# Performance work log

Hardware: AMD Instinct MI355X
Metric: run time of the kernel (lower is better)

## Reference

```python
import jax, jax.numpy as jnp
import numpy as np

B, N, C, G = 32, 1024, 64, 64

def setup_inputs() -> dict:
    key = jax.random.key(0)
    ks = jax.random.split(key, 8)
    return {
        "x": jax.random.normal(ks[0], (B, N, C), dtype=jnp.float32),
        "valid_len": jax.random.randint(ks[1], (B,), 0, N, dtype=jnp.int64) if jax.config.jax_enable_x64 else jax.random.randint(ks[1], (B,), 0, N, dtype=jnp.int32),
        "Wq": jax.random.normal(ks[2], (C, G), dtype=jnp.float32) * 0.1,
        "bq": jax.random.normal(ks[3], (G,), dtype=jnp.float32) * 0.1,
        "Wk": jax.random.normal(ks[4], (C, G), dtype=jnp.float32) * 0.1,
        "bk": jax.random.normal(ks[5], (G,), dtype=jnp.float32) * 0.1,
        "Wv": jax.random.normal(ks[6], (C, G), dtype=jnp.float32) * 0.1,
        "bv": jax.random.normal(ks[7], (G,), dtype=jnp.float32) * 0.1,
    }

def reference(x, valid_len, Wq, bq, Wk, bk, Wv, bv):
    # x: [B, N, C]; valid_len: [B] int (number of valid key positions per batch)
    q = x @ Wq + bq                                   # [B, N, G]
    k = x @ Wk + bk                                   # [B, N, G]
    v = x @ Wv + bv                                   # [B, N, G]
    scores = jnp.einsum('bnd,bmd->bnm', q, k)         # [B, N, N] (no 1/sqrt(d) scale)
    # mask: key positions >= valid_len[b] get -1e6 (matches original's -1000000.0 fill)
    col = jnp.arange(scores.shape[-1])
    mask = col[None, None, :] >= valid_len[:, None, None]
    scores = jnp.where(mask, jnp.float32(-1000000.0), scores)
    attn = jax.nn.softmax(scores, axis=-1)            # [B, N, N]
    return jnp.einsum('bnm,bmd->bnd', attn, v)        # [B, N, G]
```

## Files before the change

kernel.cpp:

```cpp
#include <hip/hip_runtime.h>
#include <stdint.h>


typedef __attribute__((ext_vector_type(4))) float    floatx4;
typedef __attribute__((ext_vector_type(8))) _Float16 halfx8;

static __device__ __forceinline__ unsigned short f2h(float f) {
    union { _Float16 h; unsigned short u; } v; v.h = (_Float16)f;
    return v.u;
}
static __device__ __forceinline__ float h2f(unsigned short u) {
    union { unsigned short u; _Float16 h; } v; v.u = u;
    return (float)v.h;
}

#define MFMA16(a, bb, c) __builtin_amdgcn_mfma_f32_16x16x32_f16((a), (bb), (c), 0, 0, 0)

#define GLD_LDS16(g, l) __builtin_amdgcn_global_load_lds(                  \
    (const __attribute__((address_space(1))) void*)(g),                    \
    (__attribute__((address_space(3))) void*)(l), 16, 0, 0)

__global__ __launch_bounds__(256, 2) void proj_kernel(
    const float* __restrict__ x,
    const float* __restrict__ Wq, const float* __restrict__ bq,
    const float* __restrict__ Wk, const float* __restrict__ bk,
    const float* __restrict__ Wv, const float* __restrict__ bv,
    unsigned short* __restrict__ qimg,
    unsigned short* __restrict__ kimg,
    unsigned short* __restrict__ vimg)
{
    __shared__ __align__(16) unsigned short sm[24576];
    const int XH = 0, XL = 4096, WQH = 8192, WQL = 12288, WKH = 16384, WVH = 20480;

    const int tid  = threadIdx.x;
    const int blk  = blockIdx.x;
    const int lane = tid & 63;
    const int w    = tid >> 6;
    const int l15  = lane & 15;
    const int quad = lane >> 4;
    const int rl   = lane >> 2;
    const int c8a  = 2 * (lane & 3);
    const int c8b  = c8a + 1;
    const int sidx_a = rl * 64 + ((c8a ^ (rl & 7)) * 8);
    const int sidx_b = rl * 64 + ((c8b ^ (rl & 7)) * 8);

    {
        const float* xrow = x + (size_t)(blk * 64 + w * 16) * 64;
#pragma unroll
        for (int i = 0; i < 2; ++i) {
            int c8   = (i == 0) ? c8a : c8b;
            int sidx = (i == 0) ? sidx_a : sidx_b;
            const float4* gp = (const float4*)(xrow + rl * 64 + c8 * 8);
            float4 f0 = gp[0], f1 = gp[1];
            float fv[8] = { f0.x, f0.y, f0.z, f0.w, f1.x, f1.y, f1.z, f1.w };
            __align__(16) unsigned short thi[8], tlo[8];
#pragma unroll
            for (int j = 0; j < 8; ++j) {
                unsigned short hi = f2h(fv[j]);
                thi[j] = hi;
                tlo[j] = f2h(fv[j] - h2f(hi));
            }
            *(uint4*)&sm[XH + w * 1024 + sidx] = *(uint4*)thi;
            *(uint4*)&sm[XL + w * 1024 + sidx] = *(uint4*)tlo;
        }
    }
    {
        int g = tid & 63, ci = tid >> 6;
#pragma unroll
        for (int j = 0; j < 16; ++j) {
            int c = ci * 16 + j;
            int idx = g * 64 + (((c >> 3) ^ (g & 7)) * 8) + (c & 7);
            float fq = Wq[c * 64 + g];
            unsigned short qhi = f2h(fq);
            sm[WQH + idx] = qhi;
            sm[WQL + idx] = f2h(fq - h2f(qhi));
            sm[WKH + idx] = f2h(Wk[c * 64 + g]);
            sm[WVH + idx] = f2h(Wv[c * 64 + g]);
        }
    }
    __syncthreads();

    const int fidx0 = l15 * 64 + (((0 + quad) ^ (l15 & 7)) * 8);
    const int fidx1 = l15 * 64 + (((4 + quad) ^ (l15 & 7)) * 8);
    halfx8 ah0 = *(const halfx8*)&sm[XH + w * 1024 + fidx0];
    halfx8 ah1 = *(const halfx8*)&sm[XH + w * 1024 + fidx1];
    halfx8 al0 = *(const halfx8*)&sm[XL + w * 1024 + fidx0];
    halfx8 al1 = *(const halfx8*)&sm[XL + w * 1024 + fidx1];

    floatx4 vacc[4];
#pragma unroll
    for (int gs = 0; gs < 4; ++gs) {
        int brow = gs * 16 + l15;
        int b0 = brow * 64 + (((0 + quad) ^ (brow & 7)) * 8);
        int b1 = brow * 64 + (((4 + quad) ^ (brow & 7)) * 8);
        halfx8 bh0 = *(const halfx8*)&sm[WQH + b0];
        halfx8 bh1 = *(const halfx8*)&sm[WQH + b1];
        halfx8 bl0 = *(const halfx8*)&sm[WQL + b0];
        halfx8 bl1 = *(const halfx8*)&sm[WQL + b1];
        halfx8 wk0 = *(const halfx8*)&sm[WKH + b0];
        halfx8 wk1 = *(const halfx8*)&sm[WKH + b1];
        halfx8 wv0 = *(const halfx8*)&sm[WVH + b0];
        halfx8 wv1 = *(const halfx8*)&sm[WVH + b1];

        float bbq = bq[gs * 16 + l15];
        floatx4 qa = { bbq, bbq, bbq, bbq };
        qa = MFMA16(ah0, bh0, qa);
        qa = MFMA16(ah1, bh1, qa);
        qa = MFMA16(ah0, bl0, qa);
        qa = MFMA16(ah1, bl1, qa);
        qa = MFMA16(al0, bh0, qa);
        qa = MFMA16(al1, bh1, qa);

        float bbk = bk[gs * 16 + l15];
        float bbv = bv[gs * 16 + l15];
        floatx4 ka = { bbk, bbk, bbk, bbk };
        floatx4 va = { bbv, bbv, bbv, bbv };
        ka = MFMA16(ah0, wk0, ka);
        ka = MFMA16(ah1, wk1, ka);
        va = MFMA16(ah0, wv0, va);
        va = MFMA16(ah1, wv1, va);
        vacc[gs] = va;

        int c8 = gs * 2 + (l15 >> 3);
#pragma unroll
        for (int r = 0; r < 4; ++r) {
            int row = w * 16 + quad * 4 + r;
            int idx = row * 64 + ((c8 ^ (row & 7)) * 8) + (l15 & 7);
            sm[XH + idx] = f2h(qa[r]);
            sm[XL + idx] = f2h(ka[r]);
        }
    }
    __syncthreads();
#pragma unroll
    for (int gs = 0; gs < 4; ++gs) {
        int g = gs * 16 + l15;
#pragma unroll
        for (int r = 0; r < 4; ++r) {
            int key = w * 16 + quad * 4 + r;
            sm[WQH + g * 64 + (((key >> 3) ^ (g & 7)) * 8) + (key & 7)] = f2h(vacc[gs][r]);
        }
    }
    __syncthreads();

    {
        const size_t tb = (size_t)blk * 4096;
#pragma unroll
        for (int i = 0; i < 2; ++i) {
            int ci = i * 256 + tid;
            *(uint4*)&qimg[tb + ci * 8] = *(const uint4*)&sm[XH  + ci * 8];
            *(uint4*)&kimg[tb + ci * 8] = *(const uint4*)&sm[XL  + ci * 8];
            *(uint4*)&vimg[tb + ci * 8] = *(const uint4*)&sm[WQH + ci * 8];
        }
    }
}

__global__ __launch_bounds__(256, 2) void attn_kernel(
    const unsigned short* __restrict__ qimg,
    const unsigned short* __restrict__ kimg,
    const unsigned short* __restrict__ vimg,
    const int* __restrict__ valid_len, float* __restrict__ out)
{
    __shared__ __align__(16) unsigned short smem[28672];
    __shared__ int sched[32];
    const int VSB = 12288, PS_OFF = 24576;

    const int tid  = threadIdx.x;
    const int blk  = blockIdx.x;
    const int lane = tid & 63;
    const int w    = tid >> 6;
    const int l15  = lane & 15;
    const int quad = lane >> 4;

    if (tid < 32) {
        int vlb = valid_len[tid];
        int ntb = (vlb == 0) ? 16 : ((vlb + 63) >> 6);
        int rank = 0;
        for (int b2 = 0; b2 < 32; ++b2) {
            int vl2 = valid_len[b2];
            int nt2 = (vl2 == 0) ? 16 : ((vl2 + 63) >> 6);
            rank += (nt2 > ntb) || (nt2 == ntb && b2 < tid);
        }
        sched[rank] = tid;
    }
    __syncthreads();

    const int b    = (blk < 256) ? sched[blk >> 4] : sched[31 - ((blk - 256) >> 4)];
    const int qt   = blk & 15;
    const int row0 = b * 1024 + qt * 64;

    const int vl    = valid_len[b];
    const int nt    = (vl == 0) ? 16 : ((vl + 63) >> 6);
    const int fullt = vl >> 6;

    const int arow = w * 16 + l15;
    const unsigned short* qb = qimg + (size_t)(b * 16 + qt) * 4096;
    halfx8 aq0 = *(const halfx8*)&qb[arow * 64 + (((0 + quad) ^ (arow & 7)) * 8)];
    halfx8 aq1 = *(const halfx8*)&qb[arow * 64 + (((4 + quad) ^ (arow & 7)) * 8)];

    const char* kbase = (const char*)kimg + (size_t)b * 131072 + w * 2048 + lane * 16;
    const char* vbase = (const char*)vimg + (size_t)b * 131072 + w * 2048 + lane * 16;

    {
        unsigned short* kd = &smem[w * 1024];
        unsigned short* vd = &smem[VSB + w * 1024];
        GLD_LDS16(kbase,        kd);
        GLD_LDS16(kbase + 1024, kd + 512);
        GLD_LDS16(vbase,        vd);
        GLD_LDS16(vbase + 1024, vd + 512);
        if (nt > 1) {
            unsigned short* kd1 = &smem[4096 + w * 1024];
            unsigned short* vd1 = &smem[VSB + 4096 + w * 1024];
            GLD_LDS16(kbase + 8192,        kd1);
            GLD_LDS16(kbase + 8192 + 1024, kd1 + 512);
            GLD_LDS16(vbase + 8192,        vd1);
            GLD_LDS16(vbase + 8192 + 1024, vd1 + 512);
        }
    }

    float m_r[4]    = { -INFINITY, -INFINITY, -INFINITY, -INFINITY };
    float l_lane[4] = { 0.f, 0.f, 0.f, 0.f };
    floatx4 o[4] = { {0,0,0,0}, {0,0,0,0}, {0,0,0,0}, {0,0,0,0} };

    int cur = 0;
    for (int t = 0; t < nt; ++t) {
        if (t + 1 < nt) asm volatile("s_waitcnt vmcnt(4)" ::: "memory");
        else            asm volatile("s_waitcnt vmcnt(0)" ::: "memory");
        __builtin_amdgcn_s_barrier();
        asm volatile("" ::: "memory");

        if (t + 2 < nt) {
            int nb = cur + 2; if (nb >= 3) nb -= 3;
            unsigned short* kd = &smem[nb * 4096 + w * 1024];
            unsigned short* vd = &smem[VSB + nb * 4096 + w * 1024];
            const char* kt2 = kbase + (size_t)(t + 2) * 8192;
            const char* vt2 = vbase + (size_t)(t + 2) * 8192;
            GLD_LDS16(kt2,        kd);
            GLD_LDS16(kt2 + 1024, kd + 512);
            GLD_LDS16(vt2,        vd);
            GLD_LDS16(vt2 + 1024, vd + 512);
        }

        const int KLc = cur * 4096;
        const int VSc = VSB + cur * 4096;

        floatx4 s[4];
#pragma unroll
        for (int sub = 0; sub < 4; ++sub) {
            int krow = sub * 16 + l15;
            halfx8 bk0 = *(const halfx8*)&smem[KLc + krow * 64 + (((0 + quad) ^ (krow & 7)) * 8)];
            halfx8 bk1 = *(const halfx8*)&smem[KLc + krow * 64 + (((4 + quad) ^ (krow & 7)) * 8)];
            floatx4 acc = { 0, 0, 0, 0 };
            acc = MFMA16(aq0, bk0, acc);
            acc = MFMA16(aq1, bk1, acc);
            s[sub] = acc;
        }
        if (t >= fullt) {
#pragma unroll
            for (int sub = 0; sub < 4; ++sub) {
                int key = t * 64 + sub * 16 + l15;
                if (key >= vl) { s[sub][0] = -1e6f; s[sub][1] = -1e6f; s[sub][2] = -1e6f; s[sub][3] = -1e6f; }
            }
        }

        float p[4][4];
        float alpha[4];
#pragma unroll
        for (int r = 0; r < 4; ++r) {
            float mx = fmaxf(fmaxf(s[0][r], s[1][r]), fmaxf(s[2][r], s[3][r]));
#pragma unroll
            for (int off = 1; off < 16; off <<= 1)
                mx = fmaxf(mx, __shfl_xor(mx, off, 64));
            float mnew = fmaxf(m_r[r], mx);
            alpha[r] = __expf(m_r[r] - mnew);
            float psum = 0.f;
#pragma unroll
            for (int sub = 0; sub < 4; ++sub) {
                float pv = __expf(s[sub][r] - mnew);
                p[sub][r] = pv;
                psum += pv;
            }
            l_lane[r] = l_lane[r] * alpha[r] + psum;
            m_r[r] = mnew;
        }
#pragma unroll
        for (int gs = 0; gs < 4; ++gs) {
            o[gs][0] *= alpha[0]; o[gs][1] *= alpha[1];
            o[gs][2] *= alpha[2]; o[gs][3] *= alpha[3];
        }

        unsigned short* psw = &smem[PS_OFF + w * 1024];
#pragma unroll
        for (int sub = 0; sub < 4; ++sub) {
            int c8 = sub * 2 + (l15 >> 3);
#pragma unroll
            for (int r = 0; r < 4; ++r) {
                int row = quad * 4 + r;
                psw[row * 64 + ((c8 ^ (row & 7)) * 8) + (l15 & 7)] = f2h(p[sub][r]);
            }
        }
        halfx8 ap0 = *(const halfx8*)&psw[l15 * 64 + (((0 + quad) ^ (l15 & 7)) * 8)];
        halfx8 ap1 = *(const halfx8*)&psw[l15 * 64 + (((4 + quad) ^ (l15 & 7)) * 8)];

#pragma unroll
        for (int gs = 0; gs < 4; ++gs) {
            int grow = gs * 16 + l15;
            halfx8 bv0 = *(const halfx8*)&smem[VSc + grow * 64 + (((0 + quad) ^ (grow & 7)) * 8)];
            halfx8 bv1 = *(const halfx8*)&smem[VSc + grow * 64 + (((4 + quad) ^ (grow & 7)) * 8)];
            o[gs] = MFMA16(ap0, bv0, o[gs]);
            o[gs] = MFMA16(ap1, bv1, o[gs]);
        }

        cur = (cur == 2) ? 0 : cur + 1;
    }

    float l[4];
#pragma unroll
    for (int r = 0; r < 4; ++r) {
        float ss = l_lane[r];
#pragma unroll
        for (int off = 1; off < 16; off <<= 1)
            ss += __shfl_xor(ss, off, 64);
        l[r] = ss;
    }
#pragma unroll
    for (int gs = 0; gs < 4; ++gs) {
#pragma unroll
        for (int r = 0; r < 4; ++r) {
            int row = row0 + w * 16 + quad * 4 + r;
            out[row * 64 + gs * 16 + l15] = o[gs][r] / l[r];
        }
    }
}

__global__ __launch_bounds__(256, 2) void fused_attn_fallback(
    const float* __restrict__ x,
    const float* __restrict__ Wq, const float* __restrict__ bq,
    const float* __restrict__ Wk, const float* __restrict__ bk,
    const float* __restrict__ Wv, const float* __restrict__ bv,
    const int* __restrict__ valid_len, float* __restrict__ out)
{
    __shared__ __align__(16) unsigned short smem[28672];
    __shared__ int sched[32];

    const int Q_OFF = 0, XH_OFF = 4096, KL0_OFF = 8192, KL1_OFF = 12288,
              VS0_OFF = 16384, VS1_OFF = 20480, PS_OFF = 24576;

    const int tid  = threadIdx.x;
    const int blk  = blockIdx.x;
    const int lane = tid & 63;
    const int w    = tid >> 6;
    const int l15  = lane & 15;
    const int quad = lane >> 4;

    if (tid < 32) {
        int vlb = valid_len[tid];
        int ntb = (vlb == 0) ? 16 : ((vlb + 63) >> 6);
        int rank = 0;
        for (int b2 = 0; b2 < 32; ++b2) {
            int vl2 = valid_len[b2];
            int nt2 = (vl2 == 0) ? 16 : ((vl2 + 63) >> 6);
            rank += (nt2 > ntb) || (nt2 == ntb && b2 < tid);
        }
        sched[rank] = tid;
    }
    __syncthreads();

    const int hv   = (blk < 256);
    const int b    = hv ? sched[blk >> 4] : sched[31 - ((blk - 256) >> 4)];
    const int n0   = (blk & 15) * 64;
    const int row0 = b * 1024 + n0;

    const int xsl  = XH_OFF + w * 1024;
    const int fidx0 = l15 * 64 + (((0 + quad) ^ (l15 & 7)) * 8);
    const int fidx1 = l15 * 64 + (((4 + quad) ^ (l15 & 7)) * 8);
    const int rl   = lane >> 2;
    const int c8a  = 2 * (lane & 3);
    const int c8b  = 2 * (lane & 3) + 1;
    const int sidx_a = rl * 64 + ((c8a ^ (rl & 7)) * 8);
    const int sidx_b = rl * 64 + ((c8b ^ (rl & 7)) * 8);

    const int vl    = valid_len[b];
    const int nt    = (vl == 0) ? 16 : ((vl + 63) >> 6);
    const int fullt = vl >> 6;

    {
        const float* xrow = x + (size_t)(row0 + w * 16) * 64;
#pragma unroll
        for (int i = 0; i < 2; ++i) {
            int c8 = (i == 0) ? c8a : c8b;
            int sidx = (i == 0) ? sidx_a : sidx_b;
            const float4* gp = (const float4*)(xrow + rl * 64 + c8 * 8);
            float4 f0 = gp[0], f1 = gp[1];
            float fv[8] = { f0.x, f0.y, f0.z, f0.w, f1.x, f1.y, f1.z, f1.w };
            __align__(16) unsigned short thi[8], tlo[8];
#pragma unroll
            for (int j = 0; j < 8; ++j) {
                unsigned short hi = f2h(fv[j]);
                thi[j] = hi;
                tlo[j] = f2h(fv[j] - h2f(hi));
            }
            *(uint4*)&smem[xsl + sidx]                = *(uint4*)thi;
            *(uint4*)&smem[VS0_OFF + w * 1024 + sidx] = *(uint4*)tlo;
        }
    }
    {
        int g = tid & 63, ci = tid >> 6;
#pragma unroll
        for (int j = 0; j < 16; ++j) {
            int c = ci * 16 + j;
            int idx = g * 64 + (((c >> 3) ^ (g & 7)) * 8) + (c & 7);
            float fq = Wq[c * 64 + g];
            unsigned short qhi = f2h(fq);
            smem[KL0_OFF + idx] = qhi;
            smem[KL1_OFF + idx] = f2h(fq - h2f(qhi));
            smem[VS1_OFF + idx] = f2h(Wk[c * 64 + g]);
            smem[PS_OFF  + idx] = f2h(Wv[c * 64 + g]);
        }
    }
    __syncthreads();

    halfx8 wkf0[4], wkf1[4], wvf0[4], wvf1[4];
#pragma unroll
    for (int gs = 0; gs < 4; ++gs) {
        int brow = gs * 16 + l15;
        int b0 = brow * 64 + (((0 + quad) ^ (brow & 7)) * 8);
        int b1 = brow * 64 + (((4 + quad) ^ (brow & 7)) * 8);
        wkf0[gs] = *(const halfx8*)&smem[VS1_OFF + b0];
        wkf1[gs] = *(const halfx8*)&smem[VS1_OFF + b1];
        wvf0[gs] = *(const halfx8*)&smem[PS_OFF + b0];
        wvf1[gs] = *(const halfx8*)&smem[PS_OFF + b1];
    }

    {
        halfx8 ah0 = *(const halfx8*)&smem[xsl + fidx0];
        halfx8 ah1 = *(const halfx8*)&smem[xsl + fidx1];
        halfx8 al0 = *(const halfx8*)&smem[VS0_OFF + w * 1024 + fidx0];
        halfx8 al1 = *(const halfx8*)&smem[VS0_OFF + w * 1024 + fidx1];
#pragma unroll
        for (int gs = 0; gs < 4; ++gs) {
            int brow = gs * 16 + l15;
            float bb = bq[gs * 16 + l15];
            floatx4 acc = { bb, bb, bb, bb };
            int b0 = brow * 64 + (((0 + quad) ^ (brow & 7)) * 8);
            int b1 = brow * 64 + (((4 + quad) ^ (brow & 7)) * 8);
            halfx8 bh0 = *(const halfx8*)&smem[KL0_OFF + b0];
            halfx8 bh1 = *(const halfx8*)&smem[KL0_OFF + b1];
            halfx8 bl0 = *(const halfx8*)&smem[KL1_OFF + b0];
            halfx8 bl1 = *(const halfx8*)&smem[KL1_OFF + b1];
            acc = MFMA16(ah0, bh0, acc);
            acc = MFMA16(ah1, bh1, acc);
            acc = MFMA16(ah0, bl0, acc);
            acc = MFMA16(ah1, bl1, acc);
            acc = MFMA16(al0, bh0, acc);
            acc = MFMA16(al1, bh1, acc);
            int c8 = gs * 2 + (l15 >> 3);
#pragma unroll
            for (int r = 0; r < 4; ++r) {
                int row = w * 16 + quad * 4 + r;
                smem[Q_OFF + row * 64 + ((c8 ^ (row & 7)) * 8) + (l15 & 7)] = f2h(acc[r]);
            }
        }
    }
    const int arow = w * 16 + l15;
    halfx8 aq0 = *(const halfx8*)&smem[Q_OFF + arow * 64 + (((0 + quad) ^ (arow & 7)) * 8)];
    halfx8 aq1 = *(const halfx8*)&smem[Q_OFF + arow * 64 + (((4 + quad) ^ (arow & 7)) * 8)];

    {
        const float* xrow = x + (size_t)(b * 1024 + w * 16) * 64;
#pragma unroll
        for (int i = 0; i < 2; ++i) {
            int c8 = (i == 0) ? c8a : c8b;
            int sidx = (i == 0) ? sidx_a : sidx_b;
            const float4* gp = (const float4*)(xrow + rl * 64 + c8 * 8);
            float4 f0 = gp[0], f1 = gp[1];
            __align__(16) unsigned short thi[8] = {
                f2h(f0.x), f2h(f0.y), f2h(f0.z), f2h(f0.w),
                f2h(f1.x), f2h(f1.y), f2h(f1.z), f2h(f1.w) };
            *(uint4*)&smem[xsl + sidx] = *(uint4*)thi;
        }
    }
    __syncthreads();

    {
        halfx8 kxh0 = *(const halfx8*)&smem[xsl + fidx0];
        halfx8 kxh1 = *(const halfx8*)&smem[xsl + fidx1];
#pragma unroll
        for (int gs = 0; gs < 4; ++gs) {
            float bbk = bk[gs * 16 + l15];
            float bbv = bv[gs * 16 + l15];
            floatx4 kacc = { bbk, bbk, bbk, bbk };
            floatx4 vacc = { bbv, bbv, bbv, bbv };
            kacc = MFMA16(kxh0, wkf0[gs], kacc);
            kacc = MFMA16(kxh1, wkf1[gs], kacc);
            vacc = MFMA16(kxh0, wvf0[gs], vacc);
            vacc = MFMA16(kxh1, wvf1[gs], vacc);
            int c8 = gs * 2 + (l15 >> 3);
            int g  = gs * 16 + l15;
#pragma unroll
            for (int r = 0; r < 4; ++r) {
                int key = w * 16 + quad * 4 + r;
                smem[KL0_OFF + key * 64 + ((c8 ^ (key & 7)) * 8) + (l15 & 7)] = f2h(kacc[r]);
                smem[VS0_OFF + g * 64 + (((key >> 3) ^ (g & 7)) * 8) + (key & 7)] = f2h(vacc[r]);
            }
        }
    }

    float m_r[4]    = { -INFINITY, -INFINITY, -INFINITY, -INFINITY };
    float l_lane[4] = { 0.f, 0.f, 0.f, 0.f };
    floatx4 o[4] = { {0,0,0,0}, {0,0,0,0}, {0,0,0,0}, {0,0,0,0} };

    for (int t = 0; t < nt; ++t) {
        bool pre = (t + 1) < nt;
        float4 pfa0, pfa1, pfb0, pfb1;
        if (pre) {
            const float* xrow = x + (size_t)(b * 1024 + (t + 1) * 64 + w * 16) * 64;
            pfa0 = ((const float4*)(xrow + rl * 64 + c8a * 8))[0];
            pfa1 = ((const float4*)(xrow + rl * 64 + c8a * 8))[1];
            pfb0 = ((const float4*)(xrow + rl * 64 + c8b * 8))[0];
            pfb1 = ((const float4*)(xrow + rl * 64 + c8b * 8))[1];
        }
        __syncthreads();

        if (pre) {
            __align__(16) unsigned short ta[8] = {
                f2h(pfa0.x), f2h(pfa0.y), f2h(pfa0.z), f2h(pfa0.w),
                f2h(pfa1.x), f2h(pfa1.y), f2h(pfa1.z), f2h(pfa1.w) };
            __align__(16) unsigned short tb[8] = {
                f2h(pfb0.x), f2h(pfb0.y), f2h(pfb0.z), f2h(pfb0.w),
                f2h(pfb1.x), f2h(pfb1.y), f2h(pfb1.z), f2h(pfb1.w) };
            *(uint4*)&smem[xsl + sidx_a] = *(uint4*)ta;
            *(uint4*)&smem[xsl + sidx_b] = *(uint4*)tb;
            halfx8 kxh0 = *(const halfx8*)&smem[xsl + fidx0];
            halfx8 kxh1 = *(const halfx8*)&smem[xsl + fidx1];
            const int KLn = ((t + 1) & 1) ? KL1_OFF : KL0_OFF;
            const int VSn = ((t + 1) & 1) ? VS1_OFF : VS0_OFF;
#pragma unroll
            for (int gs = 0; gs < 4; ++gs) {
                float bbk = bk[gs * 16 + l15];
                float bbv = bv[gs * 16 + l15];
                floatx4 kacc = { bbk, bbk, bbk, bbk };
                floatx4 vacc = { bbv, bbv, bbv, bbv };
                kacc = MFMA16(kxh0, wkf0[gs], kacc);
                kacc = MFMA16(kxh1, wkf1[gs], kacc);
                vacc = MFMA16(kxh0, wvf0[gs], vacc);
                vacc = MFMA16(kxh1, wvf1[gs], vacc);
                int c8 = gs * 2 + (l15 >> 3);
                int g  = gs * 16 + l15;
#pragma unroll
                for (int r = 0; r < 4; ++r) {
                    int key = w * 16 + quad * 4 + r;
                    smem[KLn + key * 64 + ((c8 ^ (key & 7)) * 8) + (l15 & 7)] = f2h(kacc[r]);
                    smem[VSn + g * 64 + (((key >> 3) ^ (g & 7)) * 8) + (key & 7)] = f2h(vacc[r]);
                }
            }
        }

        const int KLc = (t & 1) ? KL1_OFF : KL0_OFF;
        const int VSc = (t & 1) ? VS1_OFF : VS0_OFF;

        floatx4 s[4];
#pragma unroll
        for (int sub = 0; sub < 4; ++sub) {
            int krow = sub * 16 + l15;
            halfx8 bk0 = *(const halfx8*)&smem[KLc + krow * 64 + (((0 + quad) ^ (krow & 7)) * 8)];
            halfx8 bk1 = *(const halfx8*)&smem[KLc + krow * 64 + (((4 + quad) ^ (krow & 7)) * 8)];
            floatx4 acc = { 0, 0, 0, 0 };
            acc = MFMA16(aq0, bk0, acc);
            acc = MFMA16(aq1, bk1, acc);
            s[sub] = acc;
        }
        if (t >= fullt) {
#pragma unroll
            for (int sub = 0; sub < 4; ++sub) {
                int key = t * 64 + sub * 16 + l15;
                if (key >= vl) { s[sub][0] = -1e6f; s[sub][1] = -1e6f; s[sub][2] = -1e6f; s[sub][3] = -1e6f; }
            }
        }

        float p[4][4];
        float alpha[4];
#pragma unroll
        for (int r = 0; r < 4; ++r) {
            float mx = fmaxf(fmaxf(s[0][r], s[1][r]), fmaxf(s[2][r], s[3][r]));
#pragma unroll
            for (int off = 1; off < 16; off <<= 1)
                mx = fmaxf(mx, __shfl_xor(mx, off, 64));
            float mnew = fmaxf(m_r[r], mx);
            alpha[r] = __expf(m_r[r] - mnew);
            float psum = 0.f;
#pragma unroll
            for (int sub = 0; sub < 4; ++sub) {
                float pv = __expf(s[sub][r] - mnew);
                p[sub][r] = pv;
                psum += pv;
            }
            l_lane[r] = l_lane[r] * alpha[r] + psum;
            m_r[r] = mnew;
        }
#pragma unroll
        for (int gs = 0; gs < 4; ++gs) {
            o[gs][0] *= alpha[0]; o[gs][1] *= alpha[1];
            o[gs][2] *= alpha[2]; o[gs][3] *= alpha[3];
        }

        unsigned short* psw = &smem[PS_OFF + w * 1024];
#pragma unroll
        for (int sub = 0; sub < 4; ++sub) {
            int c8 = sub * 2 + (l15 >> 3);
#pragma unroll
            for (int r = 0; r < 4; ++r) {
                int row = quad * 4 + r;
                psw[row * 64 + ((c8 ^ (row & 7)) * 8) + (l15 & 7)] = f2h(p[sub][r]);
            }
        }
        halfx8 ap0 = *(const halfx8*)&psw[fidx0];
        halfx8 ap1 = *(const halfx8*)&psw[fidx1];

#pragma unroll
        for (int gs = 0; gs < 4; ++gs) {
            int grow = gs * 16 + l15;
            halfx8 bv0 = *(const halfx8*)&smem[VSc + grow * 64 + (((0 + quad) ^ (grow & 7)) * 8)];
            halfx8 bv1 = *(const halfx8*)&smem[VSc + grow * 64 + (((4 + quad) ^ (grow & 7)) * 8)];
            o[gs] = MFMA16(ap0, bv0, o[gs]);
            o[gs] = MFMA16(ap1, bv1, o[gs]);
        }
    }

    float l[4];
#pragma unroll
    for (int r = 0; r < 4; ++r) {
        float ss = l_lane[r];
#pragma unroll
        for (int off = 1; off < 16; off <<= 1)
            ss += __shfl_xor(ss, off, 64);
        l[r] = ss;
    }
#pragma unroll
    for (int gs = 0; gs < 4; ++gs) {
#pragma unroll
        for (int r = 0; r < 4; ++r) {
            int row = row0 + w * 16 + quad * 4 + r;
            out[row * 64 + gs * 16 + l15] = o[gs][r] / l[r];
        }
    }
}

extern "C" void kernel_launch(void* const* d_in, const int* in_sizes, int n_in,
                              void* d_out, int out_size, void* d_ws, size_t ws_size,
                              hipStream_t stream) {
    const float* x    = (const float*)d_in[0];
    const int*   vlen = (const int*)  d_in[1];
    const float* Wq   = (const float*)d_in[2];
    const float* bq   = (const float*)d_in[3];
    const float* Wk   = (const float*)d_in[4];
    const float* bk   = (const float*)d_in[5];
    const float* Wv   = (const float*)d_in[6];
    const float* bv   = (const float*)d_in[7];
    float* out = (float*)d_out;

    const size_t IMG_SHORTS = (size_t)32 * 16 * 4096;
    const size_t NEED = 3 * IMG_SHORTS * sizeof(unsigned short);

    if (ws_size >= NEED) {
        unsigned short* qimg = (unsigned short*)d_ws;
        unsigned short* kimg = qimg + IMG_SHORTS;
        unsigned short* vimg = kimg + IMG_SHORTS;
        proj_kernel<<<512, 256, 0, stream>>>(x, Wq, bq, Wk, bk, Wv, bv,
                                             qimg, kimg, vimg);
        attn_kernel<<<512, 256, 0, stream>>>(qimg, kimg, vimg, vlen, out);
    } else {
        fused_attn_fallback<<<512, 256, 0, stream>>>(
            x, Wq, bq, Wk, bk, Wv, bv, vlen, out);
    }
}
```

Baseline: 106.1 us.

## Load K/V tiles directly into registers instead of LDS triple-buffering

Replaces the async global-to-LDS triple-buffered K/V pipeline, with its per-tile barriers, by direct global loads of the swizzled K/V fragments into registers. The next K tile is prefetched into registers and V is loaded at the start of each iteration. This removes the block-wide barriers and the LDS traffic, and cuts shared memory to the P staging buffer, which may allow more resident blocks. In exchange it raises register pressure and puts global-load latency on the critical path, and each wave now reads all of K/V from L2 separately.

```diff
diff --git a/kernel.cpp b/kernel.cpp
--- a/kernel.cpp
+++ b/kernel.cpp
@@ -15,10 +15,6 @@
 }
 
 #define MFMA16(a, bb, c) __builtin_amdgcn_mfma_f32_16x16x32_f16((a), (bb), (c), 0, 0, 0)
-
-#define GLD_LDS16(g, l) __builtin_amdgcn_global_load_lds(                  \
-    (const __attribute__((address_space(1))) void*)(g),                    \
-    (__attribute__((address_space(3))) void*)(l), 16, 0, 0)
 
 __global__ __launch_bounds__(256, 2) void proj_kernel(
     const float* __restrict__ x,
@@ -160,9 +156,8 @@
     const unsigned short* __restrict__ vimg,
     const int* __restrict__ valid_len, float* __restrict__ out)
 {
-    __shared__ __align__(16) unsigned short smem[28672];
+    __shared__ __align__(16) unsigned short psmem[4096];
     __shared__ int sched[32];
-    const int VSB = 12288, PS_OFF = 24576;
 
     const int tid  = threadIdx.x;
     const int blk  = blockIdx.x;
@@ -197,63 +192,59 @@
     halfx8 aq0 = *(const halfx8*)&qb[arow * 64 + (((0 + quad) ^ (arow & 7)) * 8)];
     halfx8 aq1 = *(const halfx8*)&qb[arow * 64 + (((4 + quad) ^ (arow & 7)) * 8)];
 
-    const char* kbase = (const char*)kimg + (size_t)b * 131072 + w * 2048 + lane * 16;
-    const char* vbase = (const char*)vimg + (size_t)b * 131072 + w * 2048 + lane * 16;
-
-    {
-        unsigned short* kd = &smem[w * 1024];
-        unsigned short* vd = &smem[VSB + w * 1024];
-        GLD_LDS16(kbase,        kd);
-        GLD_LDS16(kbase + 1024, kd + 512);
-        GLD_LDS16(vbase,        vd);
-        GLD_LDS16(vbase + 1024, vd + 512);
-        if (nt > 1) {
-            unsigned short* kd1 = &smem[4096 + w * 1024];
-            unsigned short* vd1 = &smem[VSB + 4096 + w * 1024];
-            GLD_LDS16(kbase + 8192,        kd1);
-            GLD_LDS16(kbase + 8192 + 1024, kd1 + 512);
-            GLD_LDS16(vbase + 8192,        vd1);
-            GLD_LDS16(vbase + 8192 + 1024, vd1 + 512);
-        }
-    }
+    int idx0[4], idx1[4];
+#pragma unroll
+    for (int sub = 0; sub < 4; ++sub) {
+        int r = sub * 16 + l15;
+        idx0[sub] = r * 64 + (((0 + quad) ^ (r & 7)) * 8);
+        idx1[sub] = r * 64 + (((4 + quad) ^ (r & 7)) * 8);
+    }
+
+    const unsigned short* kt_base = kimg + (size_t)b * 65536;
+    const unsigned short* vt_base = vimg + (size_t)b * 65536;
 
     float m_r[4]    = { -INFINITY, -INFINITY, -INFINITY, -INFINITY };
     float l_lane[4] = { 0.f, 0.f, 0.f, 0.f };
     floatx4 o[4] = { {0,0,0,0}, {0,0,0,0}, {0,0,0,0}, {0,0,0,0} };
 
-    int cur = 0;
+    unsigned short* psw = &psmem[w * 1024];
+
+    halfx8 kf0[4], kf1[4];
+#pragma unroll
+    for (int sub = 0; sub < 4; ++sub) {
+        kf0[sub] = *(const halfx8*)&kt_base[idx0[sub]];
+        kf1[sub] = *(const halfx8*)&kt_base[idx1[sub]];
+    }
+
     for (int t = 0; t < nt; ++t) {
-        if (t + 1 < nt) asm volatile("s_waitcnt vmcnt(4)" ::: "memory");
-        else            asm volatile("s_waitcnt vmcnt(0)" ::: "memory");
-        __builtin_amdgcn_s_barrier();
-        asm volatile("" ::: "memory");
-
-        if (t + 2 < nt) {
-            int nb = cur + 2; if (nb >= 3) nb -= 3;
-            unsigned short* kd = &smem[nb * 4096 + w * 1024];
-            unsigned short* vd = &smem[VSB + nb * 4096 + w * 1024];
-            const char* kt2 = kbase + (size_t)(t + 2) * 8192;
-            const char* vt2 = vbase + (size_t)(t + 2) * 8192;
-            GLD_LDS16(kt2,        kd);
-            GLD_LDS16(kt2 + 1024, kd + 512);
-            GLD_LDS16(vt2,        vd);
-            GLD_LDS16(vt2 + 1024, vd + 512);
-        }
-
-        const int KLc = cur * 4096;
-        const int VSc = VSB + cur * 4096;
+        const unsigned short* vt = vt_base + (size_t)t * 4096;
+        halfx8 vf0[4], vf1[4];
+#pragma unroll
+        for (int sub = 0; sub < 4; ++sub) {
+            vf0[sub] = *(const halfx8*)&vt[idx0[sub]];
+            vf1[sub] = *(const halfx8*)&vt[idx1[sub]];
+        }
 
         floatx4 s[4];
 #pragma unroll
         for (int sub = 0; sub < 4; ++sub) {
-            int krow = sub * 16 + l15;
-            halfx8 bk0 = *(const halfx8*)&smem[KLc + krow * 64 + (((0 + quad) ^ (krow & 7)) * 8)];
-            halfx8 bk1 = *(const halfx8*)&smem[KLc + krow * 64 + (((4 + quad) ^ (krow & 7)) * 8)];
             floatx4 acc = { 0, 0, 0, 0 };
-            acc = MFMA16(aq0, bk0, acc);
-            acc = MFMA16(aq1, bk1, acc);
+            acc = MFMA16(aq0, kf0[sub], acc);
+            acc = MFMA16(aq1, kf1[sub], acc);
             s[sub] = acc;
         }
+
+        const bool pre = (t + 1) < nt;
+        halfx8 nk0[4], nk1[4];
+        if (pre) {
+            const unsigned short* ktn = kt_base + (size_t)(t + 1) * 4096;
+#pragma unroll
+            for (int sub = 0; sub < 4; ++sub) {
+                nk0[sub] = *(const halfx8*)&ktn[idx0[sub]];
+                nk1[sub] = *(const halfx8*)&ktn[idx1[sub]];
+            }
+        }
+
         if (t >= fullt) {
 #pragma unroll
             for (int sub = 0; sub < 4; ++sub) {
@@ -288,7 +279,6 @@
             o[gs][2] *= alpha[2]; o[gs][3] *= alpha[3];
         }
 
-        unsigned short* psw = &smem[PS_OFF + w * 1024];
 #pragma unroll
         for (int sub = 0; sub < 4; ++sub) {
             int c8 = sub * 2 + (l15 >> 3);
@@ -303,14 +293,17 @@
 
 #pragma unroll
         for (int gs = 0; gs < 4; ++gs) {
-            int grow = gs * 16 + l15;
-            halfx8 bv0 = *(const halfx8*)&smem[VSc + grow * 64 + (((0 + quad) ^ (grow & 7)) * 8)];
-            halfx8 bv1 = *(const halfx8*)&smem[VSc + grow * 64 + (((4 + quad) ^ (grow & 7)) * 8)];
-            o[gs] = MFMA16(ap0, bv0, o[gs]);
-            o[gs] = MFMA16(ap1, bv1, o[gs]);
-        }
-
-        cur = (cur == 2) ? 0 : cur + 1;
+            o[gs] = MFMA16(ap0, vf0[gs], o[gs]);
+            o[gs] = MFMA16(ap1, vf1[gs], o[gs]);
+        }
+
+        if (pre) {
+#pragma unroll
+            for (int sub = 0; sub < 4; ++sub) {
+                kf0[sub] = nk0[sub];
+                kf1[sub] = nk1[sub];
+            }
+        }
     }
 
     float l[4];
```

Result: faster. 99.11 us (-6.5%).
